# Performance work log

Hardware: AMD Instinct MI355X
Metric: run time of the kernel (lower is better)

## Reference

```python
import jax, jax.numpy as jnp
import numpy as np
import math

B, S, D, H, HD, DC, FF, E, K = 4, 2048, 576, 9, 64, 64, 1536, 8, 2
EPS = 1e-6


def _rms(x):
    # RMSNorm with weight=ones (module instantiates a fresh RMSNorm in forward)
    return x / jnp.sqrt(jnp.mean(x * x, axis=-1, keepdims=True) + EPS)


def _expert(h, wa, wb, wc):
    return (jax.nn.gelu(h @ wa, approximate=False) * (h @ wc)) @ wb


def _forward(x, q_w, kv_w, o_w, gate_w, w1, w2, w3, sw1, sw2, sw3):
    # ---------------- MLA ----------------
    xn = _rms(x)
    q = (xn @ q_w).reshape(B, S, H, HD)
    kv = (xn @ kv_w).reshape(B, S, H, 2 * DC)
    k, v = kv[..., :DC], kv[..., DC:]
    # RoPE (complex-pair form) applied to q only, as in the source
    theta = 1.0 / (10000.0 ** (jnp.arange(0, HD, 2, dtype=jnp.float32) / HD))
    freqs = jnp.arange(S, dtype=jnp.float32)[:, None] * theta[None, :]  # [S, HD/2]
    cos = jnp.cos(freqs)[None, :, None, :]
    sin = jnp.sin(freqs)[None, :, None, :]
    qp = q.reshape(B, S, H, HD // 2, 2)
    qe, qo = qp[..., 0], qp[..., 1]
    q = jnp.stack([qe * cos - qo * sin, qe * sin + qo * cos], axis=-1).reshape(B, S, H, HD)
    # NOTE: source matmul attends head-vs-head per token: [B,S,H,HD] x [B,S,DC,H] -> [B,S,H,H]
    attn = jnp.einsum('bshd,bstd->bsht', q, k) / math.sqrt(HD)
    attn = jax.nn.softmax(attn, axis=-1)
    ao = jnp.einsum('bsht,bstd->bshd', attn, v)  # [B,S,H,DC]
    # faithful to torch: transpose(1,2).contiguous().view(B,S,D)
    ao = ao.transpose(0, 2, 1, 3).reshape(B, S, D)
    x = ao @ o_w + x
    # ---------------- MoE ----------------
    xn = _rms(x)
    gw = jax.nn.softmax(xn @ gate_w, axis=-1)  # [B,S,E]
    tw, ti = jax.lax.top_k(gw, K)
    tw = tw / jnp.sum(tw, axis=-1, keepdims=True)
    # combine weights per expert: zero for unselected experts (same math as masked loop)
    comb = jnp.sum(tw[..., None] * jax.nn.one_hot(ti, E, dtype=x.dtype), axis=-2)  # [B,S,E]
    h1 = jax.nn.gelu(jnp.einsum('bsd,edf->ebsf', xn, w1), approximate=False)
    h3 = jnp.einsum('bsd,edf->ebsf', xn, w3)
    eo = jnp.einsum('ebsf,efd->ebsd', h1 * h3, w2)  # [E,B,S,D]
    moe_out = jnp.einsum('ebsd,bse->bsd', eo, comb)
    shared = _expert(xn, sw1, sw2, sw3)
    return moe_out + shared + x


def setup_inputs() -> dict:
    key = jax.random.key(0)
    ks = jax.random.split(key, 11)
    s = 0.02
    return {
        'x': jax.random.normal(ks[0], (B, S, D), dtype=jnp.float32),
        'q_w': jax.random.normal(ks[1], (D, D), dtype=jnp.float32) * s,
        'kv_w': jax.random.normal(ks[2], (D, H * 2 * DC), dtype=jnp.float32) * s,
        'o_w': jax.random.normal(ks[3], (D, D), dtype=jnp.float32) * s,
        'gate_w': jax.random.normal(ks[4], (D, E), dtype=jnp.float32) * s,
        'w1': jax.random.normal(ks[5], (E, D, FF), dtype=jnp.float32) * s,
        'w2': jax.random.normal(ks[6], (E, FF, D), dtype=jnp.float32) * s,
        'w3': jax.random.normal(ks[7], (E, D, FF), dtype=jnp.float32) * s,
        'sw1': jax.random.normal(ks[8], (D, FF), dtype=jnp.float32) * s,
        'sw2': jax.random.normal(ks[9], (FF, D), dtype=jnp.float32) * s,
        'sw3': jax.random.normal(ks[10], (D, FF), dtype=jnp.float32) * s,
    }


def reference(x, q_w, kv_w, o_w, gate_w, w1, w2, w3, sw1, sw2, sw3):
    return _forward(x, q_w, kv_w, o_w, gate_w, w1, w2, w3, sw1, sw2, sw3)
```

## Files before the change

kernel.cpp:

```cpp
#include <hip/hip_runtime.h>
#include <math.h>

#define B_  4
#define S_  2048
#define D_  576
#define H_  9
#define HD_ 64
#define FF_ 1536
#define E_  8
#define TOK (B_*S_)
#define T1ROWS 17408
#define T1ALL  25600

typedef unsigned int   u32x4  __attribute__((ext_vector_type(4)));
typedef unsigned short u16x8  __attribute__((ext_vector_type(8)));
typedef __bf16         bf16x8 __attribute__((ext_vector_type(8)));
typedef _Float16       f16x8  __attribute__((ext_vector_type(8)));
typedef float          f32x4  __attribute__((ext_vector_type(4)));

__device__ __forceinline__ float b2f(unsigned short u) {
    union { unsigned int i; float f; } v; v.i = ((unsigned int)u) << 16; return v.f;
}
__device__ __forceinline__ unsigned short f2b(float f) {
    unsigned int u = __builtin_bit_cast(unsigned int, f);
    unsigned int r = 0x7fffu + ((u >> 16) & 1u);
    return (unsigned short)((u + r) >> 16);
}


__global__ __launch_bounds__(256)
void rmsnorm_k(const float* __restrict__ x, unsigned short* __restrict__ xn) {
    int tok = blockIdx.x, tid = threadIdx.x;
    const float* xr = x + (size_t)tok * D_;
    float v0 = xr[tid];
    float v1 = xr[tid + 256];
    float v2 = (tid < D_ - 512) ? xr[tid + 512] : 0.f;
    float ss = v0*v0 + v1*v1 + v2*v2;
    #pragma unroll
    for (int d = 1; d < 64; d <<= 1) ss += __shfl_xor(ss, d, 64);
    __shared__ float red[4];
    if ((tid & 63) == 0) red[tid >> 6] = ss;
    __syncthreads();
    float tot = red[0] + red[1] + red[2] + red[3];
    float rms = rsqrtf(tot / (float)D_ + 1e-6f);
    unsigned short* orow = xn + (size_t)tok * D_;
    orow[tid]       = f2b(v0 * rms);
    orow[tid + 256] = f2b(v1 * rms);
    if (tid < D_ - 512) orow[tid + 512] = f2b(v2 * rms);
}

__global__ __launch_bounds__(256)
void rms32_k(const float* __restrict__ x, float* __restrict__ xn) {
    int tok = blockIdx.x, tid = threadIdx.x;
    const float* xr = x + (size_t)tok * D_;
    float v0 = xr[tid];
    float v1 = xr[tid + 256];
    float v2 = (tid < D_ - 512) ? xr[tid + 512] : 0.f;
    float ss = v0*v0 + v1*v1 + v2*v2;
    #pragma unroll
    for (int d = 1; d < 64; d <<= 1) ss += __shfl_xor(ss, d, 64);
    __shared__ float red[4];
    if ((tid & 63) == 0) red[tid >> 6] = ss;
    __syncthreads();
    float tot = red[0] + red[1] + red[2] + red[3];
    float rms = rsqrtf(tot / (float)D_ + 1e-6f);
    float* orow = xn + (size_t)tok * D_;
    orow[tid]       = v0 * rms;
    orow[tid + 256] = v1 * rms;
    if (tid < D_ - 512) orow[tid + 512] = v2 * rms;
}

__global__ __launch_bounds__(256)
void rmssplit_k(const float* __restrict__ x,
                _Float16* __restrict__ xh, _Float16* __restrict__ xl) {
    int tok = blockIdx.x, tid = threadIdx.x;
    const float* xr = x + (size_t)tok * D_;
    float v0 = xr[tid];
    float v1 = xr[tid + 256];
    float v2 = (tid < D_ - 512) ? xr[tid + 512] : 0.f;
    float ss = v0*v0 + v1*v1 + v2*v2;
    #pragma unroll
    for (int d = 1; d < 64; d <<= 1) ss += __shfl_xor(ss, d, 64);
    __shared__ float red[4];
    if ((tid & 63) == 0) red[tid >> 6] = ss;
    __syncthreads();
    float tot = red[0] + red[1] + red[2] + red[3];
    float rms = rsqrtf(tot / (float)D_ + 1e-6f);
    _Float16* hr = xh + (size_t)tok * D_;
    _Float16* lr = xl + (size_t)tok * D_;
    {
        float v = v0 * rms; _Float16 h = (_Float16)v;
        hr[tid] = h; lr[tid] = (_Float16)((v - (float)h) * 2048.0f);
    }
    {
        float v = v1 * rms; _Float16 h = (_Float16)v;
        hr[tid + 256] = h; lr[tid + 256] = (_Float16)((v - (float)h) * 2048.0f);
    }
    if (tid < D_ - 512) {
        float v = v2 * rms; _Float16 h = (_Float16)v;
        hr[tid + 512] = h; lr[tid + 512] = (_Float16)((v - (float)h) * 2048.0f);
    }
}

__global__ __launch_bounds__(256)
void convw13_k(const float* __restrict__ w1, const float* __restrict__ w3,
               const float* __restrict__ sw1, const float* __restrict__ sw3,
               unsigned short* __restrict__ wt1, unsigned short* __restrict__ wt3)
{
    const size_t WE = (size_t)D_ * FF_;
    int z = blockIdx.z;
    const float* s; unsigned short* d;
    if (z < 8)       { s = w1 + (size_t)z * WE;       d = wt1 + (size_t)z * WE; }
    else if (z == 8) { s = sw1;                        d = wt1 + 8 * WE; }
    else if (z < 17) { s = w3 + (size_t)(z - 9) * WE;  d = wt3 + (size_t)(z - 9) * WE; }
    else             { s = sw3;                        d = wt3 + 8 * WE; }
    const int K = D_, N = FF_;
    __shared__ unsigned short t[64][72];
    int n0 = blockIdx.x * 64, k0 = blockIdx.y * 64;
    int tx = threadIdx.x & 63, ty = threadIdx.x >> 6;
    #pragma unroll
    for (int i = 0; i < 16; ++i) {
        int k = i * 4 + ty;
        t[k][tx] = f2b(s[(size_t)(k0 + k) * N + n0 + tx]);
    }
    __syncthreads();
    int r = threadIdx.x >> 3, c8 = (threadIdx.x & 7) * 8;
    #pragma unroll
    for (int it = 0; it < 2; ++it, r += 32) {
        u16x8 v;
        #pragma unroll
        for (int j = 0; j < 8; ++j) v[j] = t[c8 + j][r];
        *(u16x8*)&d[(size_t)(n0 + r) * K + k0 + c8] = v;
    }
}

__global__ __launch_bounds__(256)
void convw2_k(const float* __restrict__ w2, const float* __restrict__ sw2,
              unsigned short* __restrict__ wt2)
{
    const size_t WE = (size_t)D_ * FF_;
    int z = blockIdx.z;
    const float* s = (z < 8) ? w2 + (size_t)z * WE : sw2;
    unsigned short* d = wt2 + (size_t)z * WE;
    const int K = FF_, N = D_;
    __shared__ unsigned short t[64][72];
    int n0 = blockIdx.x * 64, k0 = blockIdx.y * 64;
    int tx = threadIdx.x & 63, ty = threadIdx.x >> 6;
    #pragma unroll
    for (int i = 0; i < 16; ++i) {
        int k = i * 4 + ty;
        t[k][tx] = f2b(s[(size_t)(k0 + k) * N + n0 + tx]);
    }
    __syncthreads();
    int r = threadIdx.x >> 3, c8 = (threadIdx.x & 7) * 8;
    #pragma unroll
    for (int it = 0; it < 2; ++it, r += 32) {
        u16x8 v;
        #pragma unroll
        for (int j = 0; j < 8; ++j) v[j] = t[c8 + j][r];
        *(u16x8*)&d[(size_t)(n0 + r) * K + k0 + c8] = v;
    }
}

__global__ __launch_bounds__(256)
void convS_k(const float* __restrict__ src,
             _Float16* __restrict__ dh, _Float16* __restrict__ dl,
             int K, int N)
{
    __shared__ _Float16 th[64][72], tl[64][72];
    int n0 = blockIdx.x * 64, k0 = blockIdx.y * 64;
    int tx = threadIdx.x & 63, ty = threadIdx.x >> 6;
    #pragma unroll
    for (int i = 0; i < 16; ++i) {
        int k = i * 4 + ty;
        float v = src[(size_t)(k0 + k) * N + n0 + tx];
        _Float16 h = (_Float16)v;
        th[k][tx] = h;
        tl[k][tx] = (_Float16)((v - (float)h) * 2048.0f);
    }
    __syncthreads();
    int r = threadIdx.x >> 3, c8 = (threadIdx.x & 7) * 8;
    #pragma unroll
    for (int it = 0; it < 2; ++it, r += 32) {
        f16x8 vh, vl;
        #pragma unroll
        for (int j = 0; j < 8; ++j) { vh[j] = th[c8 + j][r]; vl[j] = tl[c8 + j][r]; }
        *(f16x8*)&dh[(size_t)(n0 + r) * K + k0 + c8] = vh;
        *(f16x8*)&dl[(size_t)(n0 + r) * K + k0 + c8] = vl;
    }
}

template<int BN, int EPI, int WB, int AB>
__global__ __launch_bounds__(256)
void gemmS_k(const float* __restrict__ A,
             const _Float16* __restrict__ Ahp, const _Float16* __restrict__ Alp,
             const float* __restrict__ Bm,
             const _Float16* __restrict__ Bhp, const _Float16* __restrict__ Blp,
             float* __restrict__ Cout, const float* __restrict__ resid,
             int M, int N, int K, int ldb)
{
    constexpr int BM = 128, BK = 64;
    constexpr int WM = BM / 2, WN = BN / 2, MI = WM / 16, NJ = WN / 16;
    __shared__ alignas(16) _Float16 Ah[BM][BK], Al[BM][BK];
    __shared__ alignas(16) _Float16 Bh[BN][BK], Bl[BN][BK];
    const int tid  = threadIdx.x;
    const int bn0  = blockIdx.x * BN, bm0 = blockIdx.y * BM;
    const int lane = tid & 63, wave = tid >> 6;
    const int l    = lane & 15, quad = lane >> 4;
    const int wm   = wave >> 1, wn = wave & 1;
    const int rsz  = (l & 7) << 3;

    f32x4 accH[MI][NJ], accL[MI][NJ];
    #pragma unroll
    for (int mi = 0; mi < MI; ++mi)
        #pragma unroll
        for (int nj = 0; nj < NJ; ++nj) {
            accH[mi][nj] = (f32x4){0.f, 0.f, 0.f, 0.f};
            accL[mi][nj] = (f32x4){0.f, 0.f, 0.f, 0.f};
        }

    const int nK = K / BK;
    for (int kc = 0; kc < nK; ++kc) {
        __syncthreads();
        if constexpr (AB == 1) {
            #pragma unroll
            for (int i = 0; i < (BM * BK) / 2048; ++i) {
                int u = i * 256 + tid;
                int r = u >> 3, c8 = (u & 7) * 8;
                int cs = c8 ^ ((r & 7) << 3);
                *(f16x8*)&Ah[r][cs] =
                    *(const f16x8*)(Ahp + (size_t)(bm0 + r) * K + kc * BK + c8);
                *(f16x8*)&Al[r][cs] =
                    *(const f16x8*)(Alp + (size_t)(bm0 + r) * K + kc * BK + c8);
            }
        } else {
            #pragma unroll
            for (int i = 0; i < (BM * BK) / 2048; ++i) {
                int u = i * 256 + tid;
                int r = u >> 3, c8 = (u & 7) * 8;
                int cs = c8 ^ ((r & 7) << 3);
                const float* ga = A + (size_t)(bm0 + r) * K + kc * BK + c8;
                f16x8 hh, ll;
                #pragma unroll
                for (int j = 0; j < 8; ++j) {
                    float v = ga[j];
                    _Float16 h = (_Float16)v;
                    hh[j] = h;
                    ll[j] = (_Float16)((v - (float)h) * 2048.0f);
                }
                *(f16x8*)&Ah[r][cs] = hh;
                *(f16x8*)&Al[r][cs] = ll;
            }
        }
        if constexpr (WB == 1) {
            #pragma unroll
            for (int i = 0; i < (BN * BK) / 2048; ++i) {
                int u = i * 256 + tid;
                int n = u >> 3, c8 = (u & 7) * 8;
                int cs = c8 ^ ((n & 7) << 3);
                *(f16x8*)&Bh[n][cs] =
                    *(const f16x8*)(Bhp + (size_t)(bn0 + n) * K + kc * BK + c8);
                *(f16x8*)&Bl[n][cs] =
                    *(const f16x8*)(Blp + (size_t)(bn0 + n) * K + kc * BK + c8);
            }
        } else {
            #pragma unroll
            for (int i = 0; i < (BN * BK) / 2048; ++i) {
                int u = i * 256 + tid;
                int n = u % BN, k8 = (u / BN) * 8;
                int cs = k8 ^ ((n & 7) << 3);
                const float* gB = Bm + (size_t)(kc * BK + k8) * ldb + bn0 + n;
                f16x8 hh, ll;
                #pragma unroll
                for (int j = 0; j < 8; ++j) {
                    float v = gB[(size_t)j * ldb];
                    _Float16 h = (_Float16)v;
                    hh[j] = h;
                    ll[j] = (_Float16)((v - (float)h) * 2048.0f);
                }
                *(f16x8*)&Bh[n][cs] = hh;
                *(f16x8*)&Bl[n][cs] = ll;
            }
        }
        __syncthreads();
        #pragma unroll
        for (int ks = 0; ks < BK; ks += 32) {
            f16x8 ah[MI], al[MI], bh[NJ], bl[NJ];
            int col = (ks + quad * 8) ^ rsz;
            #pragma unroll
            for (int mi = 0; mi < MI; ++mi) {
                ah[mi] = *(const f16x8*)&Ah[wm * WM + mi * 16 + l][col];
                al[mi] = *(const f16x8*)&Al[wm * WM + mi * 16 + l][col];
            }
            #pragma unroll
            for (int nj = 0; nj < NJ; ++nj) {
                bh[nj] = *(const f16x8*)&Bh[wn * WN + nj * 16 + l][col];
                bl[nj] = *(const f16x8*)&Bl[wn * WN + nj * 16 + l][col];
            }
            #pragma unroll
            for (int mi = 0; mi < MI; ++mi)
                #pragma unroll
                for (int nj = 0; nj < NJ; ++nj) {
                    accH[mi][nj] = __builtin_amdgcn_mfma_f32_16x16x32_f16(
                        ah[mi], bh[nj], accH[mi][nj], 0, 0, 0);
                    accL[mi][nj] = __builtin_amdgcn_mfma_f32_16x16x32_f16(
                        ah[mi], bl[nj], accL[mi][nj], 0, 0, 0);
                    accL[mi][nj] = __builtin_amdgcn_mfma_f32_16x16x32_f16(
                        al[mi], bh[nj], accL[mi][nj], 0, 0, 0);
                }
        }
    }
    #pragma unroll
    for (int mi = 0; mi < MI; ++mi)
        #pragma unroll
        for (int nj = 0; nj < NJ; ++nj)
            #pragma unroll
            for (int r = 0; r < 4; ++r) {
                int row = bm0 + wm * WM + mi * 16 + quad * 4 + r;
                int col = bn0 + wn * WN + nj * 16 + l;
                float v = accH[mi][nj][r] + accL[mi][nj][r] * (1.0f / 2048.0f);
                size_t idx = (size_t)row * N + col;
                if constexpr (EPI == 0) Cout[idx] = v;
                else                    Cout[idx] = v + resid[idx];
            }
}

__global__ __launch_bounds__(256, 2)
void gemm13_k(const unsigned short* __restrict__ A,
              const unsigned short* __restrict__ B1,
              const unsigned short* __restrict__ B3,
              unsigned short* __restrict__ T1o,
              const int* __restrict__ eidx,
              const int* __restrict__ counts,
              const int* __restrict__ offs,
              int N, long long bstr)
{
    constexpr int BM = 128, BK = 64;
    constexpr int MI = 4, NJ = 4;
    __shared__ alignas(16) unsigned short As[BM][BK];
    __shared__ alignas(16) unsigned short Bs1[BM][BK];
    __shared__ alignas(16) unsigned short Bs3[BM][BK];
    __shared__ int rowbuf[BM];
    const int tid  = threadIdx.x;
    const int bn0  = blockIdx.x * 128, bm0 = blockIdx.y * 128;
    const int lane = tid & 63, wave = tid >> 6;
    const int l    = lane & 15, quad = lane >> 4;
    const int wm   = wave >> 1, wn = wave & 1;
    const int rs   = tid >> 3, c8 = (tid & 7) * 8;
    const int wsz  = (rs & 7) << 3;
    const int rsz  = (l & 7) << 3;

    int e = blockIdx.z;
    int cnt = counts[e];
    if (bm0 >= cnt) return;
    int crow0 = offs[e];
    B1 += (long long)e * bstr;
    B3 += (long long)e * bstr;
    if (tid < BM) {
        int rr = bm0 + tid;
        rowbuf[tid] = (rr < cnt) ? eidx[e * TOK + rr] : 0;
    }
    __syncthreads();

    f32x4 acc1[MI][NJ], acc3[MI][NJ];
    #pragma unroll
    for (int mi = 0; mi < MI; ++mi)
        #pragma unroll
        for (int nj = 0; nj < NJ; ++nj) {
            acc1[mi][nj] = (f32x4){0.f, 0.f, 0.f, 0.f};
            acc3[mi][nj] = (f32x4){0.f, 0.f, 0.f, 0.f};
        }

    const int nK = D_ / BK;
    u32x4 ra[4], rb1[4], rb3[4];
    #pragma unroll
    for (int i = 0; i < 4; ++i) {
        int r = i * 32 + rs;
        int arow = rowbuf[r];
        ra[i]  = *(const u32x4*)(A  + (size_t)arow * D_ + c8);
        rb1[i] = *(const u32x4*)(B1 + (size_t)(bn0 + r) * D_ + c8);
        rb3[i] = *(const u32x4*)(B3 + (size_t)(bn0 + r) * D_ + c8);
    }
    for (int kc = 0; kc < nK; ++kc) {
        __syncthreads();
        #pragma unroll
        for (int i = 0; i < 4; ++i) {
            int r = i * 32 + rs;
            *(u32x4*)&As[r][c8 ^ wsz]  = ra[i];
            *(u32x4*)&Bs1[r][c8 ^ wsz] = rb1[i];
            *(u32x4*)&Bs3[r][c8 ^ wsz] = rb3[i];
        }
        __syncthreads();
        if (kc + 1 < nK) {
            int ko = (kc + 1) * BK;
            #pragma unroll
            for (int i = 0; i < 4; ++i) {
                int r = i * 32 + rs;
                int arow = rowbuf[r];
                ra[i]  = *(const u32x4*)(A  + (size_t)arow * D_ + ko + c8);
                rb1[i] = *(const u32x4*)(B1 + (size_t)(bn0 + r) * D_ + ko + c8);
                rb3[i] = *(const u32x4*)(B3 + (size_t)(bn0 + r) * D_ + ko + c8);
            }
        }
        #pragma unroll
        for (int ks = 0; ks < BK; ks += 32) {
            bf16x8 af[MI], b1f[NJ], b3f[NJ];
            int col = (ks + quad * 8) ^ rsz;
            #pragma unroll
            for (int mi = 0; mi < MI; ++mi)
                af[mi] = __builtin_bit_cast(bf16x8,
                    *(const u32x4*)&As[wm * 64 + mi * 16 + l][col]);
            #pragma unroll
            for (int nj = 0; nj < NJ; ++nj) {
                b1f[nj] = __builtin_bit_cast(bf16x8,
                    *(const u32x4*)&Bs1[wn * 64 + nj * 16 + l][col]);
                b3f[nj] = __builtin_bit_cast(bf16x8,
                    *(const u32x4*)&Bs3[wn * 64 + nj * 16 + l][col]);
            }
            #pragma unroll
            for (int mi = 0; mi < MI; ++mi)
                #pragma unroll
                for (int nj = 0; nj < NJ; ++nj) {
                    acc1[mi][nj] = __builtin_amdgcn_mfma_f32_16x16x32_bf16(
                        af[mi], b1f[nj], acc1[mi][nj], 0, 0, 0);
                    acc3[mi][nj] = __builtin_amdgcn_mfma_f32_16x16x32_bf16(
                        af[mi], b3f[nj], acc3[mi][nj], 0, 0, 0);
                }
        }
    }
    #pragma unroll
    for (int mi = 0; mi < MI; ++mi)
        #pragma unroll
        for (int nj = 0; nj < NJ; ++nj)
            #pragma unroll
            for (int r = 0; r < 4; ++r) {
                int lrow = bm0 + wm * 64 + mi * 16 + quad * 4 + r;
                int col  = bn0 + wn * 64 + nj * 16 + l;
                float hv = b2f(f2b(acc1[mi][nj][r]));
                float g  = 0.5f * hv * (1.0f + erff(hv * 0.70710678118654752f));
                T1o[(size_t)(crow0 + lrow) * N + col] = f2b(g * acc3[mi][nj][r]);
            }
}

__global__ __launch_bounds__(256)
void gemm2_k(const unsigned short* __restrict__ A,
             const unsigned short* __restrict__ Bm,
             float* __restrict__ Cout,
             const float* __restrict__ wgt,
             const int* __restrict__ eidx,
             const int* __restrict__ counts,
             const int* __restrict__ offs,
             int N, int K, int ldb, long long bstr)
{
    constexpr int BM = 64, BN = 192, BK = 64;
    constexpr int MI = 2, NJ = 6;
    constexpr int AIT = (BM * BK) / 2048;
    constexpr int BIT = (BN * BK) / 2048;
    __shared__ alignas(16) unsigned short As[BM][BK];
    __shared__ alignas(16) unsigned short Bs[BN][BK];
    __shared__ int rowbuf[BM];
    const int tid  = threadIdx.x;
    const int bn0  = blockIdx.x * BN, bm0 = blockIdx.y * BM;
    const int lane = tid & 63, wave = tid >> 6;
    const int l    = lane & 15, quad = lane >> 4;
    const int wm   = wave >> 1, wn = wave & 1;
    const int rs   = tid >> 3, c8 = (tid & 7) * 8;
    const int wsz  = (rs & 7) << 3;
    const int rsz  = (l & 7) << 3;

    int e = blockIdx.z;
    int cnt = counts[e];
    if (bm0 >= cnt) return;
    int crow0 = offs[e];
    int ebase = e * TOK;
    const unsigned short* Bt = Bm + (long long)e * bstr;
    if (tid < BM) {
        int rr = bm0 + tid;
        rowbuf[tid] = (rr < cnt) ? eidx[ebase + rr] : 0;
    }

    f32x4 acc[MI][NJ];
    #pragma unroll
    for (int mi = 0; mi < MI; ++mi)
        #pragma unroll
        for (int nj = 0; nj < NJ; ++nj) acc[mi][nj] = (f32x4){0.f, 0.f, 0.f, 0.f};

    const int nK = K / BK;
    u32x4 pa[AIT], pb[BIT];
    #pragma unroll
    for (int i = 0; i < AIT; ++i) {
        int r = i * 32 + rs;
        pa[i] = *(const u32x4*)(A + (size_t)(crow0 + bm0 + r) * K + c8);
    }
    #pragma unroll
    for (int i = 0; i < BIT; ++i) {
        int n = i * 32 + rs;
        pb[i] = *(const u32x4*)(Bt + (size_t)(bn0 + n) * ldb + c8);
    }
    for (int kc = 0; kc < nK; ++kc) {
        __syncthreads();
        #pragma unroll
        for (int i = 0; i < AIT; ++i) {
            int r = i * 32 + rs;
            *(u32x4*)&As[r][c8 ^ wsz] = pa[i];
        }
        #pragma unroll
        for (int i = 0; i < BIT; ++i) {
            int n = i * 32 + rs;
            *(u32x4*)&Bs[n][c8 ^ wsz] = pb[i];
        }
        __syncthreads();
        if (kc + 1 < nK) {
            int ko = (kc + 1) * BK;
            #pragma unroll
            for (int i = 0; i < AIT; ++i) {
                int r = i * 32 + rs;
                pa[i] = *(const u32x4*)(A + (size_t)(crow0 + bm0 + r) * K + ko + c8);
            }
            #pragma unroll
            for (int i = 0; i < BIT; ++i) {
                int n = i * 32 + rs;
                pb[i] = *(const u32x4*)(Bt + (size_t)(bn0 + n) * ldb + ko + c8);
            }
        }
        #pragma unroll
        for (int ks = 0; ks < BK; ks += 32) {
            bf16x8 af[MI], bfr[NJ];
            int col = (ks + quad * 8) ^ rsz;
            #pragma unroll
            for (int mi = 0; mi < MI; ++mi)
                af[mi] = __builtin_bit_cast(bf16x8,
                    *(const u32x4*)&As[wm * 32 + mi * 16 + l][col]);
            #pragma unroll
            for (int nj = 0; nj < NJ; ++nj)
                bfr[nj] = __builtin_bit_cast(bf16x8,
                    *(const u32x4*)&Bs[wn * 96 + nj * 16 + l][col]);
            #pragma unroll
            for (int mi = 0; mi < MI; ++mi)
                #pragma unroll
                for (int nj = 0; nj < NJ; ++nj)
                    acc[mi][nj] = __builtin_amdgcn_mfma_f32_16x16x32_bf16(
                        af[mi], bfr[nj], acc[mi][nj], 0, 0, 0);
        }
    }
    #pragma unroll
    for (int mi = 0; mi < MI; ++mi)
        #pragma unroll
        for (int nj = 0; nj < NJ; ++nj)
            #pragma unroll
            for (int r = 0; r < 4; ++r) {
                int lrow = bm0 + wm * 32 + mi * 16 + quad * 4 + r;
                if (lrow < cnt) {
                    int   tok = rowbuf[lrow - bm0];
                    float sc  = wgt[ebase + lrow];
                    int   col = bn0 + wn * 96 + nj * 16 + l;
                    atomicAdd(&Cout[(size_t)tok * N + col], sc * acc[mi][nj][r]);
                }
            }
}

template<int BN, int EPI, int ROUTED, int WB>
__global__ __launch_bounds__(256)
void gemm_k(const unsigned short* __restrict__ A,
            const void* __restrict__ Bm,
            void* __restrict__ Cout,
            const void* __restrict__ resid,
            const float* __restrict__ wgt,
            const int* __restrict__ eidx,
            const int* __restrict__ counts,
            const int* __restrict__ offs,
            int M, int N, int K, int ldb, long long bstr)
{
    constexpr int BM = 128, BK = 64, LDT = BK + 8;
    constexpr int WM = BM / 2, WN = BN / 2, MI = WM / 16, NJ = WN / 16;
    constexpr int AIT = (BM * BK) / 2048, BIT = (BN * BK) / 2048;
    __shared__ alignas(16) unsigned short As[BM][LDT];
    __shared__ alignas(16) unsigned short Bs[BN][LDT];
    __shared__ int rowbuf[BM];
    const int tid  = threadIdx.x;
    const int bn0  = blockIdx.x * BN, bm0 = blockIdx.y * BM;
    const int lane = tid & 63, wave = tid >> 6;
    const int l    = lane & 15, quad = lane >> 4;
    const int wm   = wave >> 1, wn = wave & 1;

    int cnt = M, crow0 = 0, ebase = 0;
    long long boff = 0;
    if constexpr (ROUTED) {
        int e = blockIdx.z;
        cnt = counts[e];
        if (bm0 >= cnt) return;
        crow0 = offs[e];
        ebase = e * TOK;
        boff  = (long long)e * bstr;
        if (tid < BM) {
            int rr = bm0 + tid;
            rowbuf[tid] = (rr < cnt) ? eidx[ebase + rr] : 0;
        }
        __syncthreads();
    }

    f32x4 acc[MI][NJ];
    #pragma unroll
    for (int mi = 0; mi < MI; ++mi)
        #pragma unroll
        for (int nj = 0; nj < NJ; ++nj) acc[mi][nj] = (f32x4){0.f, 0.f, 0.f, 0.f};

    const int nK = K / BK;
    for (int kc = 0; kc < nK; ++kc) {
        __syncthreads();
        #pragma unroll
        for (int i = 0; i < AIT; ++i) {
            int u = i * 256 + tid;
            int r = u >> 3, c8 = (u & 7) * 8;
            int arow;
            if constexpr (ROUTED && EPI != 5) arow = rowbuf[r];
            else if constexpr (ROUTED)        arow = crow0 + bm0 + r;
            else                              arow = bm0 + r;
            *(u32x4*)&As[r][c8] =
                *(const u32x4*)(A + (size_t)arow * K + kc * BK + c8);
        }
        const float* Bf = (const float*)Bm + boff;
        #pragma unroll
        for (int i = 0; i < BIT; ++i) {
            int u = i * 256 + tid;
            int n = u % BN, k8 = (u / BN) * 8;
            const float* gB = Bf + (size_t)(kc * BK + k8) * ldb + bn0 + n;
            u16x8 tmp;
            #pragma unroll
            for (int j = 0; j < 8; ++j) tmp[j] = f2b(gB[(size_t)j * ldb]);
            *(u16x8*)&Bs[n][k8] = tmp;
        }
        __syncthreads();
        #pragma unroll
        for (int ks = 0; ks < BK; ks += 32) {
            bf16x8 af[MI], bfr[NJ];
            #pragma unroll
            for (int mi = 0; mi < MI; ++mi)
                af[mi] = __builtin_bit_cast(bf16x8,
                    *(const u32x4*)&As[wm * WM + mi * 16 + l][ks + quad * 8]);
            #pragma unroll
            for (int nj = 0; nj < NJ; ++nj)
                bfr[nj] = __builtin_bit_cast(bf16x8,
                    *(const u32x4*)&Bs[wn * WN + nj * 16 + l][ks + quad * 8]);
            #pragma unroll
            for (int mi = 0; mi < MI; ++mi)
                #pragma unroll
                for (int nj = 0; nj < NJ; ++nj)
                    acc[mi][nj] = __builtin_amdgcn_mfma_f32_16x16x32_bf16(
                        af[mi], bfr[nj], acc[mi][nj], 0, 0, 0);
        }
    }
    #pragma unroll
    for (int mi = 0; mi < MI; ++mi)
        #pragma unroll
        for (int nj = 0; nj < NJ; ++nj)
            #pragma unroll
            for (int r = 0; r < 4; ++r) {
                int lrow = bm0 + wm * WM + mi * 16 + quad * 4 + r;
                int col  = bn0 + wn * WN + nj * 16 + l;
                float v = acc[mi][nj][r];
                if constexpr (EPI == 0) {
                    ((unsigned short*)Cout)[(size_t)(crow0 + lrow) * N + col] = f2b(v);
                } else if constexpr (EPI == 3) {
                    size_t ix = (size_t)(crow0 + lrow) * N + col;
                    float hv = b2f(((const unsigned short*)resid)[ix]);
                    float g = 0.5f * hv * (1.0f + erff(hv * 0.70710678118654752f));
                    ((unsigned short*)Cout)[ix] = f2b(g * v);
                } else if constexpr (EPI == 4) {
                    ((float*)Cout)[(size_t)lrow * N + col] += v;
                } else {
                    if (lrow < cnt) {
                        int   tok = rowbuf[lrow - bm0];
                        float sc  = wgt[ebase + lrow];
                        atomicAdd(&((float*)Cout)[(size_t)tok * N + col], sc * v);
                    }
                }
            }
}

__global__ __launch_bounds__(256)
void attn32_k(const float* __restrict__ q,
              const float* __restrict__ kv,
              float* __restrict__ ao,
              int pos0)
{
    int pl   = blockIdx.x * 4 + (threadIdx.x >> 6);
    int lane = threadIdx.x & 63;
    int pos  = pos0 + pl;
    int b = pos >> 11, s = pos & 2047;

    const float* qp  = q  + (size_t)pl * 576;
    const float* kvp = kv + (size_t)pl * 1152;

    int i = lane >> 1;
    float theta = powf(10000.f, -(float)i * (1.0f / 32.0f));
    float sn, cs;
    sincosf((float)s * theta, &sn, &cs);

    float qr[H_], kr[H_], vr[H_];
    #pragma unroll
    for (int h = 0; h < H_; ++h) {
        float qv = qp[h * 64 + lane];
        float qo = __shfl_xor(qv, 1, 64);
        qr[h] = (lane & 1) ? (qo * sn + qv * cs) : (qv * cs - qo * sn);
        kr[h] = kvp[h * 128 + lane];
        vr[h] = kvp[h * 128 + 64 + lane];
    }

    #pragma unroll
    for (int h = 0; h < H_; ++h) {
        float sc[H_];
        #pragma unroll
        for (int t = 0; t < H_; ++t) {
            float p = qr[h] * kr[t];
            #pragma unroll
            for (int d = 1; d < 64; d <<= 1) p += __shfl_xor(p, d, 64);
            sc[t] = p * 0.125f;
        }
        float mx = sc[0];
        #pragma unroll
        for (int t = 1; t < H_; ++t) mx = fmaxf(mx, sc[t]);
        float ssum = 0.f;
        #pragma unroll
        for (int t = 0; t < H_; ++t) { sc[t] = __expf(sc[t] - mx); ssum += sc[t]; }
        float inv = 1.0f / ssum;
        float ov = 0.f;
        #pragma unroll
        for (int t = 0; t < H_; ++t) ov += sc[t] * vr[t];
        ao[((size_t)(b * H_ + h) * S_ + s) * 64 + lane] = ov * inv;
    }
}

__global__ __launch_bounds__(256)
void gate1_k(const float* __restrict__ x2,
             const float* __restrict__ gw,
             float* __restrict__ tw,
             int*   __restrict__ tsel)
{
    int tok  = blockIdx.x * 4 + (threadIdx.x >> 6);
    int lane = threadIdx.x & 63;
    float acc[8];
    #pragma unroll
    for (int e = 0; e < 8; ++e) acc[e] = 0.f;
    float ss = 0.f;
    for (int d = lane; d < D_; d += 64) {
        float xv = x2[(size_t)tok * D_ + d];
        ss += xv * xv;
        const float* wr = gw + (size_t)d * 8;
        #pragma unroll
        for (int e = 0; e < 8; ++e) acc[e] += xv * wr[e];
    }
    #pragma unroll
    for (int d = 1; d < 64; d <<= 1) ss += __shfl_xor(ss, d, 64);
    #pragma unroll
    for (int e = 0; e < 8; ++e)
        #pragma unroll
        for (int d = 1; d < 64; d <<= 1) acc[e] += __shfl_xor(acc[e], d, 64);
    if (lane == 0) {
        float rms = rsqrtf(ss / (float)D_ + 1e-6f);
        #pragma unroll
        for (int e = 0; e < 8; ++e) acc[e] *= rms;
        float mx = acc[0];
        #pragma unroll
        for (int e = 1; e < 8; ++e) mx = fmaxf(mx, acc[e]);
        float g[8], ssum = 0.f;
        #pragma unroll
        for (int e = 0; e < 8; ++e) { g[e] = __expf(acc[e] - mx); ssum += g[e]; }
        #pragma unroll
        for (int e = 0; e < 8; ++e) g[e] /= ssum;
        int i1 = 0;
        #pragma unroll
        for (int e = 1; e < 8; ++e) if (g[e] > g[i1]) i1 = e;
        int i2 = -1;
        #pragma unroll
        for (int e = 0; e < 8; ++e)
            if (e != i1 && (i2 < 0 || g[e] > g[i2])) i2 = e;
        float s2 = g[i1] + g[i2];
        tw[(size_t)tok * 2 + 0] = g[i1] / s2;
        tw[(size_t)tok * 2 + 1] = g[i2] / s2;
        tsel[tok] = i1 | (i2 << 8);
    }
}

__global__ __launch_bounds__(256)
void gate2_k(const int*   __restrict__ tsel,
             const float* __restrict__ tw,
             float* __restrict__ wgt,
             int*   __restrict__ eidx,
             int*   __restrict__ counts)
{
    int e    = blockIdx.x;
    int tid  = threadIdx.x;
    int lane = tid & 63, wv = tid >> 6;
    __shared__ int wtot[4];
    int base = 0;
    for (int t0 = 0; t0 < TOK; t0 += 256) {
        int tok = t0 + tid;
        int hit = 0; float w = 0.f;
        if (e == E_) { hit = 1; w = 1.0f; }
        else {
            int s = tsel[tok];
            if ((s & 255) == e)      { hit = 1; w = tw[(size_t)tok * 2 + 0]; }
            else if ((s >> 8) == e)  { hit = 1; w = tw[(size_t)tok * 2 + 1]; }
        }
        unsigned long long m = __ballot(hit);
        int pre = __popcll(m & ((1ull << lane) - 1ull));
        if (lane == 0) wtot[wv] = __popcll(m);
        __syncthreads();
        int off = base;
        for (int q = 0; q < wv; ++q) off += wtot[q];
        if (hit) {
            int p = off + pre;
            eidx[e * TOK + p] = tok;
            wgt [e * TOK + p] = w;
        }
        base += wtot[0] + wtot[1] + wtot[2] + wtot[3];
        __syncthreads();
    }
    if (tid == 0) counts[e] = base;
}

__global__ void offs_k(const int* __restrict__ counts, int* __restrict__ offs) {
    if (threadIdx.x == 0) {
        int run = 0;
        for (int e = 0; e < 9; ++e) {
            offs[e] = run;
            run += ((counts[e] + 127) >> 7) << 7;
        }
    }
}

extern "C" void kernel_launch(void* const* d_in, const int* in_sizes, int n_in,
                              void* d_out, int out_size, void* d_ws, size_t ws_size,
                              hipStream_t stream)
{
    const float* x      = (const float*)d_in[0];
    const float* q_w    = (const float*)d_in[1];
    const float* kv_w   = (const float*)d_in[2];
    const float* o_w    = (const float*)d_in[3];
    const float* gate_w = (const float*)d_in[4];
    const float* w1     = (const float*)d_in[5];
    const float* w2     = (const float*)d_in[6];
    const float* w3     = (const float*)d_in[7];
    const float* sw1    = (const float*)d_in[8];
    const float* sw2    = (const float*)d_in[9];
    const float* sw3    = (const float*)d_in[10];
    float* out = (float*)d_out;

    const size_t XN = (size_t)TOK * D_ * 2;
    char* ws = (char*)d_ws;
    unsigned short* xn16 = (unsigned short*)ws;
    float*          ao32 = (float*)(ws + XN);

    const size_t QE = (size_t)D_ * D_, KVE = (size_t)1152 * D_;
    const size_t SW = (2 * QE + KVE) * 2 * 2;
    _Float16* qwh  = (_Float16*)(ws + 3 * XN);
    _Float16* qwl  = qwh  + QE;
    _Float16* kvwh = qwl  + QE;
    _Float16* kvwl = kvwh + KVE;
    _Float16* owh  = kvwl + KVE;
    _Float16* owl  = owh  + QE;

    bool convA = true;
    int TC = -1;
    for (int pass = 0; pass < 2; ++pass) {
        size_t base = 3 * XN + (convA ? SW : 0);
        if      (base + 8*XN    <= ws_size) { TC = 1; break; }
        else if (base + 8*XN/2  <= ws_size) { TC = 2; break; }
        else if (base + 8*XN/4  <= ws_size) { TC = 4; break; }
        else if (base + 8*XN/8  <= ws_size) { TC = 8; break; }
        else if (base + 8*XN/16 <= ws_size) { TC = 16; break; }
        else if (base + 8*XN/32 <= ws_size) { TC = 32; break; }
        else if (base + 8*XN/64 <= ws_size) { TC = 64; break; }
        convA = false;
    }
    if (TC < 0) { convA = false; TC = 64; }
    const int CT = TOK / TC;
    char* chunk0 = ws + 3*XN + (convA ? SW : 0);
    _Float16* xnh  = (_Float16*)chunk0;
    _Float16* xnl  = xnh + (size_t)CT * D_;
    float*    xn32c = (float*)chunk0;
    float*    qc   = (float*)(chunk0 + (size_t)CT * D_ * 4);
    float*    kvc  = qc + (size_t)CT * D_;

    int*   counts = (int*)(ws + XN);
    int*   offs   = counts + 16;
    float* wgt    = (float*)(ws + XN + 256);
    int*   eidx   = (int*)  (ws + XN + 256 + (size_t)9 * TOK * 4);
    float* tw     = (float*)(ws + XN + 256 + (size_t)9 * TOK * 8);
    int*   tsel   = (int*)  (ws + XN + 256 + (size_t)9 * TOK * 8 + (size_t)TOK * 8);
    const size_t fixedG = XN + 256 + (size_t)9 * TOK * 8 + (size_t)TOK * 12;

    const size_t WELEM = (size_t)D_ * FF_;
    const size_t WSZ   = 27 * WELEM * 2;

    bool conv; int FC;
    if      (fixedG + WSZ + (size_t)T1ALL * FF_     * 2 <= ws_size) { conv = true;  FC = 1; }
    else if (fixedG + WSZ + (size_t)T1ALL * (FF_/2) * 2 <= ws_size) { conv = true;  FC = 2; }
    else if (fixedG + WSZ + (size_t)T1ALL * (FF_/4) * 2 <= ws_size) { conv = true;  FC = 4; }
    else if (fixedG + (size_t)T1ROWS * FF_     * 2 <= ws_size)      { conv = false; FC = 1; }
    else if (fixedG + (size_t)T1ROWS * (FF_/2) * 2 <= ws_size)      { conv = false; FC = 2; }
    else                                                            { conv = false; FC = 4; }
    const int FFc = FF_ / FC;

    unsigned short* wt1 = (unsigned short*)(ws + fixedG);
    unsigned short* wt3 = wt1 + 9 * WELEM;
    unsigned short* wt2 = wt3 + 9 * WELEM;
    unsigned short* t1  = (unsigned short*)(ws + fixedG + (conv ? WSZ : 0));

    if (convA) {
        convS_k<<<dim3(D_/64,  D_/64), 256, 0, stream>>>(q_w,  qwh,  qwl,  D_, D_);
        convS_k<<<dim3(1152/64, D_/64), 256, 0, stream>>>(kv_w, kvwh, kvwl, D_, 1152);
        convS_k<<<dim3(D_/64,  D_/64), 256, 0, stream>>>(o_w,  owh,  owl,  D_, D_);
    }
    for (int t = 0; t < TC; ++t) {
        const float* xc = x + (size_t)t * CT * D_;
        if (convA) {
            rmssplit_k<<<CT, 256, 0, stream>>>(xc, xnh, xnl);
            gemmS_k<64, 0, 1, 1><<<dim3(D_ / 64, CT / 128), 256, 0, stream>>>(
                nullptr, xnh, xnl, nullptr, qwh, qwl, qc, nullptr, CT, D_, D_, D_);
            gemmS_k<64, 0, 1, 1><<<dim3(1152 / 64, CT / 128), 256, 0, stream>>>(
                nullptr, xnh, xnl, nullptr, kvwh, kvwl, kvc, nullptr, CT, 1152, D_, D_);
        } else {
            rms32_k<<<CT, 256, 0, stream>>>(xc, xn32c);
            gemmS_k<64, 0, 0, 0><<<dim3(D_ / 64, CT / 128), 256, 0, stream>>>(
                xn32c, nullptr, nullptr, q_w, nullptr, nullptr, qc, nullptr, CT, D_, D_, D_);
            gemmS_k<64, 0, 0, 0><<<dim3(1152 / 64, CT / 128), 256, 0, stream>>>(
                xn32c, nullptr, nullptr, kv_w, nullptr, nullptr, kvc, nullptr, CT, 1152, D_, 1152);
        }
        attn32_k<<<CT / 4, 256, 0, stream>>>(qc, kvc, ao32, t * CT);
    }
    if (convA)
        gemmS_k<64, 1, 1, 0><<<dim3(D_ / 64, TOK / 128), 256, 0, stream>>>(
            ao32, nullptr, nullptr, nullptr, owh, owl, out, x, TOK, D_, D_, D_);
    else
        gemmS_k<64, 1, 0, 0><<<dim3(D_ / 64, TOK / 128), 256, 0, stream>>>(
            ao32, nullptr, nullptr, o_w, nullptr, nullptr, out, x, TOK, D_, D_, D_);
    rmsnorm_k<<<TOK, 256, 0, stream>>>(out, xn16);
    gate1_k<<<TOK / 4, 256, 0, stream>>>(out, gate_w, tw, tsel);
    gate2_k<<<E_ + 1, 256, 0, stream>>>(tsel, tw, wgt, eidx, counts);
    offs_k<<<1, 64, 0, stream>>>(counts, offs);
    if (conv) {
        convw13_k<<<dim3(FF_/64, D_/64, 18), 256, 0, stream>>>(
            w1, w3, sw1, sw3, wt1, wt3);
        convw2_k<<<dim3(D_/64, FF_/64, 9), 256, 0, stream>>>(w2, sw2, wt2);
    }
    for (int c = 0; c < FC; ++c) {
        if (conv) {
            gemm13_k<<<dim3(FFc / 128, TOK / 128, 9), 256, 0, stream>>>(
                xn16, wt1 + (size_t)c * FFc * D_, wt3 + (size_t)c * FFc * D_,
                t1, eidx, counts, offs, FFc, (long long)WELEM);
            gemm2_k<<<dim3(D_ / 192, TOK / 64, 9), 256, 0, stream>>>(
                t1, wt2 + (size_t)c * FFc, out, wgt, eidx, counts, offs,
                D_, FFc, FF_, (long long)WELEM);
        } else {
            const float* w1c = w1 + (size_t)c * FFc;
            const float* w3c = w3 + (size_t)c * FFc;
            const float* w2c = w2 + (size_t)c * FFc * D_;
            gemm_k<128, 0, 1, 0><<<dim3(FFc / 128, TOK / 128, E_), 256, 0, stream>>>(
                xn16, w1c, t1, nullptr, wgt, eidx, counts, offs,
                TOK, FFc, D_, FF_, (long long)D_ * FF_);
            gemm_k<128, 3, 1, 0><<<dim3(FFc / 128, TOK / 128, E_), 256, 0, stream>>>(
                xn16, w3c, t1, t1, wgt, eidx, counts, offs,
                TOK, FFc, D_, FF_, (long long)D_ * FF_);
            gemm_k<64, 5, 1, 0><<<dim3(D_ / 64, TOK / 128, E_), 256, 0, stream>>>(
                t1, w2c, out, nullptr, wgt, eidx, counts, offs,
                TOK, D_, FFc, D_, (long long)FF_ * D_);
            gemm_k<128, 0, 0, 0><<<dim3(FFc / 128, TOK / 128), 256, 0, stream>>>(
                xn16, sw1 + (size_t)c * FFc, t1, nullptr, nullptr, nullptr, nullptr, nullptr,
                TOK, FFc, D_, FF_, 0);
            gemm_k<128, 3, 0, 0><<<dim3(FFc / 128, TOK / 128), 256, 0, stream>>>(
                xn16, sw3 + (size_t)c * FFc, t1, t1, nullptr, nullptr, nullptr, nullptr,
                TOK, FFc, D_, FF_, 0);
            gemm_k<64, 4, 0, 0><<<dim3(D_ / 64, TOK / 128), 256, 0, stream>>>(
                t1, sw2 + (size_t)c * FFc * D_, out, nullptr, nullptr, nullptr, nullptr, nullptr,
                TOK, D_, FFc, D_, 0);
        }
    }
}
```

Before: 621.1 us.

## Flatten MoE grids over padded expert rows, merge weight conversions, emit split-f16 attention output

The grouped MoE GEMMs no longer launch a 3D grid with one z-slice per expert. They launch a flat grid over padded expert rows, and each block finds its expert by scanning the counts, which removes the offs_k launch and the many early-exit blocks. The three attention-weight conversion launches are merged into one kernel indexed by blockIdx.z. The attention kernel now writes hi/lo f16 split output directly, so the output projection takes its split-A path and skips the fp32 intermediate. Risks: the row padding to 128 must match how t1 is laid out, and gemm2 (BM=64) uses the 128-padded base.

```diff
diff --git a/kernel.cpp b/kernel.cpp
--- a/kernel.cpp
+++ b/kernel.cpp
@@ -163,10 +163,18 @@
 }
 
 __global__ __launch_bounds__(256)
-void convS_k(const float* __restrict__ src,
-             _Float16* __restrict__ dh, _Float16* __restrict__ dl,
-             int K, int N)
+void convSall_k(const float* __restrict__ q_w, const float* __restrict__ kv_w,
+                const float* __restrict__ o_w,
+                _Float16* __restrict__ qwh,  _Float16* __restrict__ qwl,
+                _Float16* __restrict__ kvwh, _Float16* __restrict__ kvwl,
+                _Float16* __restrict__ owh,  _Float16* __restrict__ owl)
 {
+    int z = blockIdx.z;
+    const float* src; _Float16 *dh, *dl; int N;
+    if (z == 0)      { if (blockIdx.x >= D_/64) return; src = q_w;  dh = qwh;  dl = qwl;  N = D_; }
+    else if (z == 1) { src = kv_w; dh = kvwh; dl = kvwl; N = 1152; }
+    else             { if (blockIdx.x >= D_/64) return; src = o_w;  dh = owh;  dl = owl;  N = D_; }
+    const int K = D_;
     __shared__ _Float16 th[64][72], tl[64][72];
     int n0 = blockIdx.x * 64, k0 = blockIdx.y * 64;
     int tx = threadIdx.x & 63, ty = threadIdx.x >> 6;
@@ -332,7 +340,6 @@
               unsigned short* __restrict__ T1o,
               const int* __restrict__ eidx,
               const int* __restrict__ counts,
-              const int* __restrict__ offs,
               int N, long long bstr)
 {
     constexpr int BM = 128, BK = 64;
@@ -342,7 +349,6 @@
     __shared__ alignas(16) unsigned short Bs3[BM][BK];
     __shared__ int rowbuf[BM];
     const int tid  = threadIdx.x;
-    const int bn0  = blockIdx.x * 128, bm0 = blockIdx.y * 128;
     const int lane = tid & 63, wave = tid >> 6;
     const int l    = lane & 15, quad = lane >> 4;
     const int wm   = wave >> 1, wn = wave & 1;
@@ -350,10 +356,18 @@
     const int wsz  = (rs & 7) << 3;
     const int rsz  = (l & 7) << 3;
 
-    int e = blockIdx.z;
-    int cnt = counts[e];
-    if (bm0 >= cnt) return;
-    int crow0 = offs[e];
+    int row0 = blockIdx.y * BM;
+    int e = 0, base = 0;
+    for (; e < 9; ++e) {
+        int pc = ((counts[e] + 127) >> 7) << 7;
+        if (row0 < base + pc) break;
+        base += pc;
+    }
+    if (e >= 9) return;
+    int cnt   = counts[e];
+    int bm0   = row0 - base;
+    int crow0 = base;
+    const int bn0 = blockIdx.x * 128;
     B1 += (long long)e * bstr;
     B3 += (long long)e * bstr;
     if (tid < BM) {
@@ -449,7 +463,6 @@
              const float* __restrict__ wgt,
              const int* __restrict__ eidx,
              const int* __restrict__ counts,
-             const int* __restrict__ offs,
              int N, int K, int ldb, long long bstr)
 {
     constexpr int BM = 64, BN = 192, BK = 64;
@@ -460,7 +473,6 @@
     __shared__ alignas(16) unsigned short Bs[BN][BK];
     __shared__ int rowbuf[BM];
     const int tid  = threadIdx.x;
-    const int bn0  = blockIdx.x * BN, bm0 = blockIdx.y * BM;
     const int lane = tid & 63, wave = tid >> 6;
     const int l    = lane & 15, quad = lane >> 4;
     const int wm   = wave >> 1, wn = wave & 1;
@@ -468,11 +480,19 @@
     const int wsz  = (rs & 7) << 3;
     const int rsz  = (l & 7) << 3;
 
-    int e = blockIdx.z;
-    int cnt = counts[e];
-    if (bm0 >= cnt) return;
-    int crow0 = offs[e];
+    int row0 = blockIdx.y * BM;
+    int e = 0, base = 0;
+    for (; e < 9; ++e) {
+        int pc = ((counts[e] + 127) >> 7) << 7;
+        if (row0 < base + pc) break;
+        base += pc;
+    }
+    if (e >= 9) return;
+    int cnt   = counts[e];
+    int bm0   = row0 - base;
+    int crow0 = base;
     int ebase = e * TOK;
+    const int bn0 = blockIdx.x * BN;
     const unsigned short* Bt = Bm + (long long)e * bstr;
     if (tid < BM) {
         int rr = bm0 + tid;
@@ -681,7 +701,8 @@
 __global__ __launch_bounds__(256)
 void attn32_k(const float* __restrict__ q,
               const float* __restrict__ kv,
-              float* __restrict__ ao,
+              _Float16* __restrict__ aoh,
+              _Float16* __restrict__ aol,
               int pos0)
 {
     int pl   = blockIdx.x * 4 + (threadIdx.x >> 6);
@@ -727,7 +748,11 @@
         float ov = 0.f;
         #pragma unroll
         for (int t = 0; t < H_; ++t) ov += sc[t] * vr[t];
-        ao[((size_t)(b * H_ + h) * S_ + s) * 64 + lane] = ov * inv;
+        float v = ov * inv;
+        size_t idx = ((size_t)(b * H_ + h) * S_ + s) * 64 + lane;
+        _Float16 hh = (_Float16)v;
+        aoh[idx] = hh;
+        aol[idx] = (_Float16)((v - (float)hh) * 2048.0f);
     }
 }
 
@@ -850,7 +875,8 @@
     const size_t XN = (size_t)TOK * D_ * 2;
     char* ws = (char*)d_ws;
     unsigned short* xn16 = (unsigned short*)ws;
-    float*          ao32 = (float*)(ws + XN);
+    _Float16* aoh = (_Float16*)(ws + XN);
+    _Float16* aol = (_Float16*)(ws + 2 * XN);
 
     const size_t QE = (size_t)D_ * D_, KVE = (size_t)1152 * D_;
     const size_t SW = (2 * QE + KVE) * 2 * 2;
@@ -909,9 +935,8 @@
     unsigned short* t1  = (unsigned short*)(ws + fixedG + (conv ? WSZ : 0));
 
     if (convA) {
-        convS_k<<<dim3(D_/64,  D_/64), 256, 0, stream>>>(q_w,  qwh,  qwl,  D_, D_);
-        convS_k<<<dim3(1152/64, D_/64), 256, 0, stream>>>(kv_w, kvwh, kvwl, D_, 1152);
-        convS_k<<<dim3(D_/64,  D_/64), 256, 0, stream>>>(o_w,  owh,  owl,  D_, D_);
+        convSall_k<<<dim3(1152/64, D_/64, 3), 256, 0, stream>>>(
+            q_w, kv_w, o_w, qwh, qwl, kvwh, kvwl, owh, owl);
     }
     for (int t = 0; t < TC; ++t) {
         const float* xc = x + (size_t)t * CT * D_;
@@ -928,30 +953,31 @@
             gemmS_k<64, 0, 0, 0><<<dim3(1152 / 64, CT / 128), 256, 0, stream>>>(
                 xn32c, nullptr, nullptr, kv_w, nullptr, nullptr, kvc, nullptr, CT, 1152, D_, 1152);
         }
-        attn32_k<<<CT / 4, 256, 0, stream>>>(qc, kvc, ao32, t * CT);
+        attn32_k<<<CT / 4, 256, 0, stream>>>(qc, kvc, aoh, aol, t * CT);
     }
     if (convA)
-        gemmS_k<64, 1, 1, 0><<<dim3(D_ / 64, TOK / 128), 256, 0, stream>>>(
-            ao32, nullptr, nullptr, nullptr, owh, owl, out, x, TOK, D_, D_, D_);
+        gemmS_k<64, 1, 1, 1><<<dim3(D_ / 64, TOK / 128), 256, 0, stream>>>(
+            nullptr, aoh, aol, nullptr, owh, owl, out, x, TOK, D_, D_, D_);
     else
-        gemmS_k<64, 1, 0, 0><<<dim3(D_ / 64, TOK / 128), 256, 0, stream>>>(
-            ao32, nullptr, nullptr, o_w, nullptr, nullptr, out, x, TOK, D_, D_, D_);
+        gemmS_k<64, 1, 0, 1><<<dim3(D_ / 64, TOK / 128), 256, 0, stream>>>(
+            nullptr, aoh, aol, o_w, nullptr, nullptr, out, x, TOK, D_, D_, D_);
     rmsnorm_k<<<TOK, 256, 0, stream>>>(out, xn16);
     gate1_k<<<TOK / 4, 256, 0, stream>>>(out, gate_w, tw, tsel);
     gate2_k<<<E_ + 1, 256, 0, stream>>>(tsel, tw, wgt, eidx, counts);
-    offs_k<<<1, 64, 0, stream>>>(counts, offs);
     if (conv) {
         convw13_k<<<dim3(FF_/64, D_/64, 18), 256, 0, stream>>>(
             w1, w3, sw1, sw3, wt1, wt3);
         convw2_k<<<dim3(D_/64, FF_/64, 9), 256, 0, stream>>>(w2, sw2, wt2);
+    } else {
+        offs_k<<<1, 64, 0, stream>>>(counts, offs);
     }
     for (int c = 0; c < FC; ++c) {
         if (conv) {
-            gemm13_k<<<dim3(FFc / 128, TOK / 128, 9), 256, 0, stream>>>(
+            gemm13_k<<<dim3(FFc / 128, T1ALL / 128), 256, 0, stream>>>(
                 xn16, wt1 + (size_t)c * FFc * D_, wt3 + (size_t)c * FFc * D_,
-                t1, eidx, counts, offs, FFc, (long long)WELEM);
-            gemm2_k<<<dim3(D_ / 192, TOK / 64, 9), 256, 0, stream>>>(
-                t1, wt2 + (size_t)c * FFc, out, wgt, eidx, counts, offs,
+                t1, eidx, counts, FFc, (long long)WELEM);
+            gemm2_k<<<dim3(D_ / 192, T1ALL / 64), 256, 0, stream>>>(
+                t1, wt2 + (size_t)c * FFc, out, wgt, eidx, counts,
                 D_, FFc, FF_, (long long)WELEM);
         } else {
             const float* w1c = w1 + (size_t)c * FFc;
```

Result: faster. 603.4 us (-2.9%).
